# Optimization experiments

Hardware: AMD Instinct MI355X
Metric: run time of the kernel (lower is better)

Reference implementation:

```python
import jax, jax.numpy as jnp
import numpy as np

NPOINT = 1024
RADIUS = 0.2
NSAMPLE = 32


def setup_inputs() -> dict:
    key = jax.random.key(0)
    ks = jax.random.split(key, 8)
    B, N, C = 8, 8192, 64
    xyz = jax.random.uniform(ks[0], (B, N, 3), dtype=jnp.float32)
    features = jax.random.normal(ks[1], (B, N, C), dtype=jnp.float32)
    c_in = C + 3  # QueryAndGroup concatenates relative xyz with features
    s = 0.05
    w1 = jax.random.normal(ks[2], (c_in, 64), dtype=jnp.float32) * s
    b1 = jnp.zeros((64,), jnp.float32)
    w2 = jax.random.normal(ks[3], (64, 64), dtype=jnp.float32) * s
    b2 = jnp.zeros((64,), jnp.float32)
    w3 = jax.random.normal(ks[4], (64, 128), dtype=jnp.float32) * s
    b3 = jnp.zeros((128,), jnp.float32)
    return {"xyz": xyz, "features": features, "w1": w1, "b1": b1,
            "w2": w2, "b2": b2, "w3": w3, "b3": b3}


def farthest_point_sample(xyz, npoint):
    # xyz: (B, N, 3) -> (B, npoint) int32 indices
    B, N, _ = xyz.shape

    def step(carry, _):
        dist, far = carry
        centroid = jnp.take_along_axis(xyz, far[:, None, None], axis=1)  # (B,1,3)
        d = jnp.sum((xyz - centroid) ** 2, axis=-1)  # (B,N)
        dist = jnp.minimum(dist, d)
        nxt = jnp.argmax(dist, axis=-1).astype(jnp.int32)
        return (dist, nxt), far

    init = (jnp.full((B, N), 1e10, jnp.float32), jnp.zeros((B,), jnp.int32))
    _, idxs = jax.lax.scan(step, init, None, length=npoint)
    return idxs.T  # (B, npoint)


def ball_query(radius, nsample, xyz, new_xyz):
    # returns (B, S, nsample) int32 neighbor indices into N
    sq = jnp.sum((new_xyz[:, :, None, :] - xyz[:, None, :, :]) ** 2, axis=-1)  # (B,S,N)
    B, S, N = sq.shape
    idx = jnp.broadcast_to(jnp.arange(N, dtype=jnp.int32), (B, S, N))
    idx = jnp.where(sq > radius * radius, N, idx)
    idx = jnp.sort(idx, axis=-1)[:, :, :nsample]
    first = idx[:, :, :1]
    idx = jnp.where(idx == N, first, idx)  # pad with first valid index
    return idx


_gather = jax.vmap(lambda pts, idx: pts[idx])  # per-batch fancy gather


def reference(xyz, features, w1, b1, w2, b2, w3, b3):
    fps_idx = farthest_point_sample(xyz, NPOINT)
    new_xyz = _gather(xyz, fps_idx)  # (B, S, 3)
    nbr_idx = ball_query(RADIUS, NSAMPLE, xyz, new_xyz)  # (B, S, K)
    g_xyz = _gather(xyz, nbr_idx) - new_xyz[:, :, None, :]  # (B,S,K,3) relative coords
    g_feat = _gather(features, nbr_idx)  # (B, S, K, C)
    x = jnp.concatenate([g_xyz, g_feat], axis=-1)  # (B, S, K, C+3)
    # shared pointwise MLP (Conv2d 1x1 + ReLU)
    x = jax.nn.relu(x @ w1 + b1)
    x = jax.nn.relu(x @ w2 + b2)
    x = jax.nn.relu(x @ w3 + b3)
    new_features = jnp.max(x, axis=2)  # max-pool over neighbors -> (B, S, 128)
    return new_xyz, jnp.transpose(new_features, (0, 2, 1))  # (B,S,3), (B,128,S)
```

## Files before the change

kernel.cpp:

```cpp
#include <hip/hip_runtime.h>
#include <stdint.h>

#define N_PTS 8192
#define B_SZ 8
#define NPOINT_ 1024
#define NSAMPLE_ 32
#define NPROD 8
#define NCONS 240
#define CWAVES (NCONS * 8)
#define PUBK 64

typedef float __attribute__((ext_vector_type(2))) f32x2;

template <int CTRL>
__device__ __forceinline__ float dpp_maxf(float v) {
    int o = __builtin_amdgcn_update_dpp(__float_as_int(v), __float_as_int(v),
                                        CTRL, 0xf, 0xf, false);
    return fmaxf(v, __int_as_float(o));
}
template <int CTRL>
__device__ __forceinline__ int dpp_mini(int v) {
    int o = __builtin_amdgcn_update_dpp(v, v, CTRL, 0xf, 0xf, false);
    return (o < v) ? o : v;
}

__device__ __forceinline__ float ld_coh(const float* p) {
    return __int_as_float(__hip_atomic_load((int*)p, __ATOMIC_RELAXED,
                                            __HIP_MEMORY_SCOPE_AGENT));
}
__device__ __forceinline__ void st_coh(float* p, float v) {
    __hip_atomic_store((int*)p, __float_as_int(v), __ATOMIC_RELAXED,
                       __HIP_MEMORY_SCOPE_AGENT);
}

#define SM_SPTS 0
#define SM_CVAL 131072
#define SM_CIDX 131136
#define SM_W1 0
#define SM_W2 17408
#define SM_W3 33792
#define SM_B1 66560
#define SM_B2 66816
#define SM_B3 67072
#define SM_XB 67584
#define SM_HB 102400
#define SM_NIDX 137216
#define SM_TOTAL 138240

__global__ __launch_bounds__(512, 2) void fused_kernel(
    const float* __restrict__ xyz, const float* __restrict__ feat,
    const float* __restrict__ w1, const float* __restrict__ b1,
    const float* __restrict__ w2, const float* __restrict__ b2,
    const float* __restrict__ w3, const float* __restrict__ b3,
    float* __restrict__ new_xyz, float* __restrict__ out,
    int* __restrict__ prog) {
    __shared__ __align__(16) char smem[SM_TOTAL];
    const int t = threadIdx.x;
    const int wave = t >> 6, lane = t & 63;

    if (blockIdx.x < NPROD) {
        float4* spts = (float4*)smem;
        float* cval = (float*)(smem + SM_CVAL);
        int* cidx = (int*)(smem + SM_CIDX);
        const int b = blockIdx.x;
        const float* bx = xyz + (size_t)b * N_PTS * 3;
        int* pp = prog + b * 64;

        f32x2 px[8], py[8], pz[8], dst[8];
#pragma unroll
        for (int jj = 0; jj < 8; ++jj) {
            int p0 = t + 512 * (2 * jj);
            int p1 = t + 512 * (2 * jj + 1);
            float x0 = bx[3 * p0 + 0], y0 = bx[3 * p0 + 1], z0 = bx[3 * p0 + 2];
            float x1 = bx[3 * p1 + 0], y1 = bx[3 * p1 + 1], z1 = bx[3 * p1 + 2];
            spts[p0] = make_float4(x0, y0, z0, 0.0f);
            spts[p1] = make_float4(x1, y1, z1, 0.0f);
            px[jj] = f32x2{x0, x1};
            py[jj] = f32x2{y0, y1};
            pz[jj] = f32x2{z0, z1};
            dst[jj] = f32x2{1e10f, 1e10f};
        }
        __syncthreads();

        float cx = bx[0], cy = bx[1], cz = bx[2];
        if (t == 0) {
            st_coh(&new_xyz[(b * NPOINT_) * 3 + 0], cx);
            st_coh(&new_xyz[(b * NPOINT_) * 3 + 1], cy);
            st_coh(&new_xyz[(b * NPOINT_) * 3 + 2], cz);
        }

        for (int it = 1; it < NPOINT_; ++it) {
            f32x2 cx2 = f32x2{cx, cx}, cy2 = f32x2{cy, cy}, cz2 = f32x2{cz, cz};
            {
#pragma clang fp contract(off)
#pragma unroll
                for (int jj = 0; jj < 8; ++jj) {
                    f32x2 dx = px[jj] - cx2;
                    f32x2 dy = py[jj] - cy2;
                    f32x2 dz = pz[jj] - cz2;
                    f32x2 d = (dx * dx + dy * dy) + dz * dz;
                    dst[jj] = __builtin_elementwise_min(dst[jj], d);
                }
            }
            f32x2 m01 = __builtin_elementwise_max(dst[0], dst[1]);
            f32x2 m23 = __builtin_elementwise_max(dst[2], dst[3]);
            f32x2 m45 = __builtin_elementwise_max(dst[4], dst[5]);
            f32x2 m67 = __builtin_elementwise_max(dst[6], dst[7]);
            f32x2 m03 = __builtin_elementwise_max(m01, m23);
            f32x2 m47 = __builtin_elementwise_max(m45, m67);
            f32x2 mm = __builtin_elementwise_max(m03, m47);
            float bv = fmaxf(mm.x, mm.y);
            int lj = 0;
#pragma unroll
            for (int jj = 7; jj >= 0; --jj) {
                lj = (dst[jj].y == bv) ? 2 * jj + 1 : lj;
                lj = (dst[jj].x == bv) ? 2 * jj : lj;
            }
            int idx = (lj << 9) + t;

            float mv = bv;
            mv = dpp_maxf<0x111>(mv);
            mv = dpp_maxf<0x112>(mv);
            mv = dpp_maxf<0x114>(mv);
            mv = dpp_maxf<0x118>(mv);
            mv = dpp_maxf<0x142>(mv);
            mv = dpp_maxf<0x143>(mv);
            float wmax = __int_as_float(
                __builtin_amdgcn_readlane(__float_as_int(mv), 63));
            int ic = (bv == wmax) ? idx : 0x7FFFFFFF;
            ic = dpp_mini<0x111>(ic);
            ic = dpp_mini<0x112>(ic);
            ic = dpp_mini<0x114>(ic);
            ic = dpp_mini<0x118>(ic);
            ic = dpp_mini<0x142>(ic);
            ic = dpp_mini<0x143>(ic);

            const int buf = it & 1;
            if (lane == 63) {
                cval[buf * 8 + wave] = wmax;
                cidx[buf * 8 + wave] = ic;
            }
            __syncthreads();

            float cv = cval[buf * 8 + (lane & 7)];
            int ci = cidx[buf * 8 + (lane & 7)];
            float gm = cv;
            gm = dpp_maxf<0x111>(gm);
            gm = dpp_maxf<0x112>(gm);
            gm = dpp_maxf<0x114>(gm);
            float gmax =
                __int_as_float(__builtin_amdgcn_readlane(__float_as_int(gm), 7));
            int ic2 = (cv == gmax) ? ci : 0x7FFFFFFF;
            ic2 = dpp_mini<0x111>(ic2);
            ic2 = dpp_mini<0x112>(ic2);
            ic2 = dpp_mini<0x114>(ic2);
            int wi = __builtin_amdgcn_readlane(ic2, 7);

            float4 sp = spts[wi];
            cx = sp.x;
            cy = sp.y;
            cz = sp.z;
            if (t == 0) {
                st_coh(&new_xyz[(b * NPOINT_ + it) * 3 + 0], cx);
                st_coh(&new_xyz[(b * NPOINT_ + it) * 3 + 1], cy);
                st_coh(&new_xyz[(b * NPOINT_ + it) * 3 + 2], cz);
                if ((it & (PUBK - 1)) == (PUBK - 1)) {
                    __hip_atomic_store(pp, it + 1, __ATOMIC_RELEASE,
                                       __HIP_MEMORY_SCOPE_AGENT);
                }
            }
        }
    } else {
        float* lw1T = (float*)(smem + SM_W1);
        float* lw2T = (float*)(smem + SM_W2);
        float* lw3T = (float*)(smem + SM_W3);
        float* lb1 = (float*)(smem + SM_B1);
        float* lb2 = (float*)(smem + SM_B2);
        float* lb3 = (float*)(smem + SM_B3);

        for (int i = t; i < 67 * 64; i += 512) {
            int k = i >> 6, c = i & 63;
            lw1T[c * 68 + k] = w1[i];
        }
        if (t < 64) lw1T[t * 68 + 67] = 0.0f;
        for (int i = t; i < 64 * 64; i += 512) {
            int k = i >> 6, c = i & 63;
            lw2T[c * 64 + k] = w2[i];
        }
        for (int i = t; i < 64 * 128; i += 512) {
            int k = i >> 7, c = i & 127;
            lw3T[c * 64 + k] = w3[i];
        }
        if (t < 64) {
            lb1[t] = b1[t];
            lb2[t] = b2[t];
        }
        if (t < 128) lb3[t] = b3[t];
        __syncthreads();

        float* xw = (float*)(smem + SM_XB) + wave * (16 * 68);
        float* hw = (float*)(smem + SM_HB) + wave * (16 * 68);
        int* nw = (int*)(smem + SM_NIDX) + wave * 32;
        const float* wc1 = lw1T + lane * 68;
        const float* wc2 = lw2T + lane * 64;
        const float* wca = lw3T + lane * 64;
        const float* wcb = lw3T + (lane + 64) * 64;

        const int widx = (blockIdx.x - NPROD) * 8 + wave;
        for (int cc = widx; cc < B_SZ * NPOINT_; cc += CWAVES) {
            const int s = cc >> 3, b = cc & 7;
            const int g = (b << 10) + s;
            int* pp = prog + b * 64;

            int pv = __hip_atomic_load(pp, __ATOMIC_RELAXED,
                                       __HIP_MEMORY_SCOPE_AGENT);
            while (pv <= s) {
                if (s - pv >= 64)
                    __builtin_amdgcn_s_sleep(64);
                else
                    __builtin_amdgcn_s_sleep(16);
                pv = __hip_atomic_load(pp, __ATOMIC_RELAXED,
                                       __HIP_MEMORY_SCOPE_AGENT);
            }
            __builtin_amdgcn_fence(__ATOMIC_ACQUIRE, "agent");
            const float cx = ld_coh(&new_xyz[g * 3 + 0]);
            const float cy = ld_coh(&new_xyz[g * 3 + 1]);
            const float cz = ld_coh(&new_xyz[g * 3 + 2]);

            const float* bx = xyz + (size_t)b * N_PTS * 3;
            const float r2 = 0.04f;
            int taken = 0, firstIdx = -1;
            for (int ch = 0; ch < N_PTS / 64 && taken < NSAMPLE_; ++ch) {
                int p = ch * 64 + lane;
                float dxq = __fsub_rn(bx[3 * p + 0], cx);
                float dyq = __fsub_rn(bx[3 * p + 1], cy);
                float dzq = __fsub_rn(bx[3 * p + 2], cz);
                float sq = __fadd_rn(
                    __fadd_rn(__fmul_rn(dxq, dxq), __fmul_rn(dyq, dyq)),
                    __fmul_rn(dzq, dzq));
                bool pred = !(sq > r2);
                unsigned long long mask = __ballot(pred);
                if (mask) {
                    int cnt = __popcll(mask);
                    if (firstIdx < 0) firstIdx = ch * 64 + (__ffsll(mask) - 1);
                    if (pred) {
                        int pos =
                            taken + __popcll(mask & ((1ull << lane) - 1ull));
                        if (pos < NSAMPLE_) nw[pos] = p;
                    }
                    taken += cnt;
                }
            }
            if (lane >= taken && lane < NSAMPLE_) nw[lane] = firstIdx;
            asm volatile("s_waitcnt lgkmcnt(0)" ::: "memory");

            float mo0 = 0.0f, mo1 = 0.0f;
            for (int half = 0; half < 2; ++half) {
                int iis[16];
#pragma unroll
                for (int r = 0; r < 16; ++r) iis[r] = nw[half * 16 + r];
#pragma unroll
                for (int r = 0; r < 16; ++r) {
                    xw[r * 68 + 3 + lane] =
                        feat[((size_t)b * N_PTS + iis[r]) * 64 + lane];
                    if (lane < 3) {
                        float pv2 = xyz[((size_t)b * N_PTS + iis[r]) * 3 + lane];
                        float cv = (lane == 0) ? cx : ((lane == 1) ? cy : cz);
                        xw[r * 68 + lane] = pv2 - cv;
                    }
                    if (lane == 0) xw[r * 68 + 67] = 0.0f;
                }
                f32x2 acc2[16];
                {
                    float bias = lb1[lane];
#pragma unroll
                    for (int r = 0; r < 16; ++r) acc2[r] = f32x2{bias, 0.0f};
                    for (int kk = 0; kk < 68; kk += 4) {
                        f32x2 wA = *(const f32x2*)(wc1 + kk);
                        f32x2 wB = *(const f32x2*)(wc1 + kk + 2);
#pragma unroll
                        for (int r = 0; r < 16; ++r) {
                            float4 xv = *(const float4*)&xw[r * 68 + kk];
                            f32x2 xa = f32x2{xv.x, xv.y};
                            f32x2 xc = f32x2{xv.z, xv.w};
                            acc2[r] = xa * wA + acc2[r];
                            acc2[r] = xc * wB + acc2[r];
                        }
                    }
#pragma unroll
                    for (int r = 0; r < 16; ++r)
                        hw[r * 68 + lane] = fmaxf(acc2[r].x + acc2[r].y, 0.0f);
                }
                {
                    float bias = lb2[lane];
#pragma unroll
                    for (int r = 0; r < 16; ++r) acc2[r] = f32x2{bias, 0.0f};
                    for (int kk = 0; kk < 64; kk += 4) {
                        f32x2 wA = *(const f32x2*)(wc2 + kk);
                        f32x2 wB = *(const f32x2*)(wc2 + kk + 2);
#pragma unroll
                        for (int r = 0; r < 16; ++r) {
                            float4 hv = *(const float4*)&hw[r * 68 + kk];
                            f32x2 xa = f32x2{hv.x, hv.y};
                            f32x2 xc = f32x2{hv.z, hv.w};
                            acc2[r] = xa * wA + acc2[r];
                            acc2[r] = xc * wB + acc2[r];
                        }
                    }
#pragma unroll
                    for (int r = 0; r < 16; ++r)
                        xw[r * 68 + lane] = fmaxf(acc2[r].x + acc2[r].y, 0.0f);
                }
                {
                    f32x2 a2[16], c2[16];
                    float bb0 = lb3[lane], bb1 = lb3[lane + 64];
#pragma unroll
                    for (int r = 0; r < 16; ++r) {
                        a2[r] = f32x2{bb0, 0.0f};
                        c2[r] = f32x2{bb1, 0.0f};
                    }
                    for (int kk = 0; kk < 64; kk += 4) {
                        f32x2 wA0 = *(const f32x2*)(wca + kk);
                        f32x2 wB0 = *(const f32x2*)(wca + kk + 2);
                        f32x2 wA1 = *(const f32x2*)(wcb + kk);
                        f32x2 wB1 = *(const f32x2*)(wcb + kk + 2);
#pragma unroll
                        for (int r = 0; r < 16; ++r) {
                            float4 hv = *(const float4*)&xw[r * 68 + kk];
                            f32x2 xa = f32x2{hv.x, hv.y};
                            f32x2 xc = f32x2{hv.z, hv.w};
                            a2[r] = xa * wA0 + a2[r];
                            a2[r] = xc * wB0 + a2[r];
                            c2[r] = xa * wA1 + c2[r];
                            c2[r] = xc * wB1 + c2[r];
                        }
                    }
#pragma unroll
                    for (int r = 0; r < 16; ++r) {
                        mo0 = fmaxf(mo0, fmaxf(a2[r].x + a2[r].y, 0.0f));
                        mo1 = fmaxf(mo1, fmaxf(c2[r].x + c2[r].y, 0.0f));
                    }
                }
            }
            out[((size_t)b * 128 + lane) * 1024 + s] = mo0;
            out[((size_t)b * 128 + lane + 64) * 1024 + s] = mo1;
        }
    }
}

extern "C" void kernel_launch(void* const* d_in, const int* in_sizes, int n_in,
                              void* d_out, int out_size, void* d_ws,
                              size_t ws_size, hipStream_t stream) {
    const float* xyz = (const float*)d_in[0];
    const float* feat = (const float*)d_in[1];
    const float* w1 = (const float*)d_in[2];
    const float* b1 = (const float*)d_in[3];
    const float* w2 = (const float*)d_in[4];
    const float* b2 = (const float*)d_in[5];
    const float* w3 = (const float*)d_in[6];
    const float* b3 = (const float*)d_in[7];

    float* out_xyz = (float*)d_out;
    float* out_feat = (float*)d_out + B_SZ * NPOINT_ * 3;
    int* prog = (int*)d_ws;

    hipMemsetAsync(d_ws, 0, NPROD * 64 * sizeof(int), stream);
    fused_kernel<<<NPROD + NCONS, 512, 0, stream>>>(
        xyz, feat, w1, b1, w2, b2, w3, b3, out_xyz, out_feat, prog);
}
```

Baseline: 1.026 ms.

## Batch FPS centroid publishing per 64 iterations and pad weight LDS strides

```diff
diff --git a/kernel.cpp b/kernel.cpp
--- a/kernel.cpp
+++ b/kernel.cpp
@@ -8,7 +8,6 @@
 #define NPROD 8
 #define NCONS 240
 #define CWAVES (NCONS * 8)
-#define PUBK 64
 
 typedef float __attribute__((ext_vector_type(2))) f32x2;
 
@@ -37,15 +36,19 @@
 #define SM_CVAL 131072
 #define SM_CIDX 131136
 #define SM_W1 0
-#define SM_W2 17408
-#define SM_W3 33792
-#define SM_B1 66560
-#define SM_B2 66816
-#define SM_B3 67072
-#define SM_XB 67584
-#define SM_HB 102400
-#define SM_NIDX 137216
-#define SM_TOTAL 138240
+#define SM_W2 17920
+#define SM_W3 34816
+#define SM_B1 68608
+#define SM_B2 68864
+#define SM_B3 69120
+#define SM_XB 69632
+#define SM_HB 104448
+#define SM_NIDX 139264
+#define SM_TOTAL 140288
+
+#define W1S 70
+#define W2S 66
+#define W3S 66
 
 __global__ __launch_bounds__(512, 2) void fused_kernel(
     const float* __restrict__ xyz, const float* __restrict__ feat,
@@ -83,11 +86,7 @@
         __syncthreads();
 
         float cx = bx[0], cy = bx[1], cz = bx[2];
-        if (t == 0) {
-            st_coh(&new_xyz[(b * NPOINT_) * 3 + 0], cx);
-            st_coh(&new_xyz[(b * NPOINT_) * 3 + 1], cy);
-            st_coh(&new_xyz[(b * NPOINT_) * 3 + 2], cz);
-        }
+        int hold = 0;
 
         for (int it = 1; it < NPOINT_; ++it) {
             f32x2 cx2 = f32x2{cx, cx}, cy2 = f32x2{cy, cy}, cz2 = f32x2{cz, cz};
@@ -142,6 +141,11 @@
             }
             __syncthreads();
 
+            if ((it & 63) == 0 && t == 0) {
+                __hip_atomic_store(pp, it, __ATOMIC_RELAXED,
+                                   __HIP_MEMORY_SCOPE_AGENT);
+            }
+
             float cv = cval[buf * 8 + (lane & 7)];
             int ci = cidx[buf * 8 + (lane & 7)];
             float gm = cv;
@@ -156,19 +160,25 @@
             ic2 = dpp_mini<0x114>(ic2);
             int wi = __builtin_amdgcn_readlane(ic2, 7);
 
+            hold = (lane == (it & 63)) ? wi : hold;
+
             float4 sp = spts[wi];
             cx = sp.x;
             cy = sp.y;
             cz = sp.z;
-            if (t == 0) {
-                st_coh(&new_xyz[(b * NPOINT_ + it) * 3 + 0], cx);
-                st_coh(&new_xyz[(b * NPOINT_ + it) * 3 + 1], cy);
-                st_coh(&new_xyz[(b * NPOINT_ + it) * 3 + 2], cz);
-                if ((it & (PUBK - 1)) == (PUBK - 1)) {
-                    __hip_atomic_store(pp, it + 1, __ATOMIC_RELEASE,
-                                       __HIP_MEMORY_SCOPE_AGENT);
-                }
-            }
+
+            if ((it & 63) == 63 && wave == 0) {
+                float4 me = spts[hold];
+                int s0 = b * NPOINT_ + (it - 63) + lane;
+                st_coh(&new_xyz[s0 * 3 + 0], me.x);
+                st_coh(&new_xyz[s0 * 3 + 1], me.y);
+                st_coh(&new_xyz[s0 * 3 + 2], me.z);
+            }
+        }
+        __syncthreads();
+        if (t == 0) {
+            __hip_atomic_store(pp, NPOINT_, __ATOMIC_RELAXED,
+                               __HIP_MEMORY_SCOPE_AGENT);
         }
     } else {
         float* lw1T = (float*)(smem + SM_W1);
@@ -180,16 +190,16 @@
 
         for (int i = t; i < 67 * 64; i += 512) {
             int k = i >> 6, c = i & 63;
-            lw1T[c * 68 + k] = w1[i];
-        }
-        if (t < 64) lw1T[t * 68 + 67] = 0.0f;
+            lw1T[c * W1S + k] = w1[i];
+        }
+        if (t < 64) lw1T[t * W1S + 67] = 0.0f;
         for (int i = t; i < 64 * 64; i += 512) {
             int k = i >> 6, c = i & 63;
-            lw2T[c * 64 + k] = w2[i];
+            lw2T[c * W2S + k] = w2[i];
         }
         for (int i = t; i < 64 * 128; i += 512) {
             int k = i >> 7, c = i & 127;
-            lw3T[c * 64 + k] = w3[i];
+            lw3T[c * W3S + k] = w3[i];
         }
         if (t < 64) {
             lb1[t] = b1[t];
@@ -201,10 +211,10 @@
         float* xw = (float*)(smem + SM_XB) + wave * (16 * 68);
         float* hw = (float*)(smem + SM_HB) + wave * (16 * 68);
         int* nw = (int*)(smem + SM_NIDX) + wave * 32;
-        const float* wc1 = lw1T + lane * 68;
-        const float* wc2 = lw2T + lane * 64;
-        const float* wca = lw3T + lane * 64;
-        const float* wcb = lw3T + (lane + 64) * 64;
+        const float* wc1 = lw1T + lane * W1S;
+        const float* wc2 = lw2T + lane * W2S;
+        const float* wca = lw3T + lane * W3S;
+        const float* wcb = lw3T + (lane + 64) * W3S;
 
         const int widx = (blockIdx.x - NPROD) * 8 + wave;
         for (int cc = widx; cc < B_SZ * NPOINT_; cc += CWAVES) {
```

Result: no change. 1.023 ms (-0.3%).
